# Performance work log

Measured on AMD Instinct MI355X. Metric: run time of the kernel, lower is better.

## Reference

```python
import jax, jax.numpy as jnp
import numpy as np

B, T, K = 64, 1024, 128
START, STOP = K - 2, K - 1  # tag_dictionary['<START>'], tag_dictionary['<STOP>']
NEG = -10000.0


def setup_inputs() -> dict:
    key = jax.random.key(0)
    k1, k2, k3, k4 = jax.random.split(key, 4)
    feats = jax.random.normal(k1, (B, T, K), jnp.float32)
    tags = jax.random.randint(k2, (B, T), 0, K - 2)          # real labels only
    lens = jax.random.randint(k3, (B,), 1, T + 1)            # 1 <= len <= T
    transitions = jax.random.normal(k4, (K, K), jnp.float32)
    transitions = transitions.at[START, :].set(NEG).at[:, STOP].set(NEG)
    return {"feats": feats, "tags": tags, "lens": lens, "transitions": transitions}


def _forward_alg(feats, transitions, lens):
    # feats: [B, T, K]; CRF forward (log-partition) via scan over time.
    B_, T_, K_ = feats.shape
    # init: only START position kept from feats[:, 0, :], rest -10000
    alpha0 = jnp.full((B_, K_), NEG, feats.dtype).at[:, START].set(feats[:, 0, START])

    def step(alpha, feat_i):
        # tag_var[b, s, p] = feat_i[b, s] + transitions[s, p] + alpha[b, p]
        new = feat_i + jax.scipy.special.logsumexp(alpha[:, None, :] + transitions[None, :, :], axis=2)
        return new, new

    _, alphas = jax.lax.scan(step, alpha0, jnp.swapaxes(feats[:, 1:, :], 0, 1))  # [T-1, B, K]
    all_alphas = jnp.concatenate([alpha0[None], alphas], axis=0)  # [T, B, K]; idx t-1 == forward_var[:, t]
    terminal = all_alphas[lens - 1, jnp.arange(B_)]               # [B, K]
    return jax.scipy.special.logsumexp(terminal, axis=1)          # [B]


def _score_sentence(feats, transitions, tags, lens):
    B_, T_, K_ = feats.shape
    pos = jnp.arange(T_ - 1)
    # pad_stop_tags = tags[:, 1:] with positions >= len-1 replaced by STOP
    stop_tags = jnp.where(pos[None, :] >= (lens - 1)[:, None], STOP, tags[:, 1:])
    trans_sc = transitions[stop_tags, tags[:, :-1]]               # [B, T-1]
    tmask = (pos[None, :] < (lens - 1)[:, None]).astype(feats.dtype)
    emit = jnp.take_along_axis(feats, tags[:, :, None], axis=2)[:, :, 0]  # [B, T]
    emask = (jnp.arange(T_)[None, :] < lens[:, None]).astype(feats.dtype)
    return jnp.sum(trans_sc * tmask, axis=1) + jnp.sum(emit * emask, axis=1)


def reference(feats, tags, lens, transitions):
    forward_score = _forward_alg(feats, transitions, lens)
    gold_score = _score_sentence(feats, transitions, tags, lens)
    return jnp.mean(forward_score - gold_score)
```

## Files before the change

### kernel.cpp

```cpp
#include <hip/hip_runtime.h>
#include <math.h>

#define BB 64
#define TT 1024
#define KK 128
#define START_TAG 126
#define STOP_TAG 127
#define NTHREADS 256
#define CS 64
#define EP 36

typedef float v2f __attribute__((ext_vector_type(2)));

__device__ __forceinline__ float quad_add(float x) {
  int y = __builtin_amdgcn_update_dpp(0, __float_as_int(x), 0xB1, 0xF, 0xF, true);
  x = x + __int_as_float(y);
  y = __builtin_amdgcn_update_dpp(0, __float_as_int(x), 0x4E, 0xF, 0xF, true);
  return x + __int_as_float(y);
}
__device__ __forceinline__ float quad_max(float x) {
  int y = __builtin_amdgcn_update_dpp(0, __float_as_int(x), 0xB1, 0xF, 0xF, true);
  x = fmaxf(x, __int_as_float(y));
  y = __builtin_amdgcn_update_dpp(0, __float_as_int(x), 0x4E, 0xF, 0xF, true);
  return fmaxf(x, __int_as_float(y));
}

__global__ __launch_bounds__(NTHREADS) void crf_forward(
    const float* __restrict__ feats,
    const int*   __restrict__ tags,
    const int*   __restrict__ lens,
    const float* __restrict__ trans,
    float*       __restrict__ out_pb)
{
  __shared__ float Tld[KK][KK + 1];
  __shared__ __align__(16) float ebuf[2][4 * EP];
  __shared__ float sbuf[2];
  __shared__ float maxT_lds[KK];
  __shared__ __align__(16) float Fbuf[CS * KK];
  __shared__ float wsum[NTHREADS / 64];

  const int tid = threadIdx.x;
  const int b   = blockIdx.x;
  const int q   = tid & 3;
  const int g   = tid >> 2;
  const int r0  = 2 * g;
  const int L   = lens[b];
  const float* fb = feats + (size_t)b * TT * KK;

  for (int i = tid; i < KK * KK / 4; i += NTHREADS) {
    float4 v = ((const float4*)trans)[i];
    int rr = i >> 5, cc = (i & 31) * 4;
    Tld[rr][cc] = v.x; Tld[rr][cc + 1] = v.y; Tld[rr][cc + 2] = v.z; Tld[rr][cc + 3] = v.w;
  }
  __syncthreads();

  float m0 = -INFINITY, m1 = -INFINITY;
  #pragma unroll
  for (int i = 0; i < 32; ++i) {
    m0 = fmaxf(m0, Tld[r0][q * 32 + i]);
    m1 = fmaxf(m1, Tld[r0 + 1][q * 32 + i]);
  }
  m0 = quad_max(m0);
  m1 = quad_max(m1);
  v2f Ea[16], Eb[16];
  #pragma unroll
  for (int i = 0; i < 16; ++i) {
    Ea[i][0] = __expf(Tld[r0][q * 32 + 2 * i]         - m0);
    Ea[i][1] = __expf(Tld[r0][q * 32 + 2 * i + 1]     - m0);
    Eb[i][0] = __expf(Tld[r0 + 1][q * 32 + 2 * i]     - m1);
    Eb[i][1] = __expf(Tld[r0 + 1][q * 32 + 2 * i + 1] - m1);
  }
  if (q == 0) { maxT_lds[r0] = m0; maxT_lds[r0 + 1] = m1; }

  if (tid < KK)
    ebuf[0][(tid >> 5) * EP + (tid & 31)] = (tid == START_TAG) ? 1.0f : 0.0f;
  if (tid == 0) sbuf[0] = 1.0f;
  float M = fb[START_TAG];
  __syncthreads();

  const int j0 = (tid * 32) & (KK - 1);
  float4 mTv[8];
  #pragma unroll
  for (int i = 0; i < 8; ++i) mTv[i] = ((const float4*)maxT_lds)[(j0 >> 2) + i];

  float4 pf[8];
  {
    const float4* src = (const float4*)fb;
    #pragma unroll
    for (int i = 0; i < 8; ++i) pf[i] = src[tid * 8 + i];
  }

  int p = 0;
  for (int c = 0; c * CS < L; ++c) {
    float4* Fb4 = (float4*)Fbuf;
    #pragma unroll
    for (int i = 0; i < 8; ++i) {
      float4 v = pf[i], mm = mTv[i];
      float4 o;
      o.x = __expf(v.x + mm.x); o.y = __expf(v.y + mm.y);
      o.z = __expf(v.z + mm.z); o.w = __expf(v.w + mm.w);
      Fb4[tid * 8 + i] = o;
    }
    if ((c + 1) * CS < TT) {
      const float4* src = (const float4*)(fb + (size_t)(c + 1) * CS * KK);
      #pragma unroll
      for (int i = 0; i < 8; ++i) pf[i] = src[tid * 8 + i];
    }
    __syncthreads();

    const int t_begin = (c == 0) ? 1 : c * CS;
    const int t_end   = (L < (c + 1) * CS) ? L : (c + 1) * CS;
    for (int t = t_begin; t < t_end; ++t) {
      const float* er = ebuf[p];
      float* ew = ebuf[p ^ 1];
      const float sp = sbuf[p];
      const v2f Fv = *(const v2f*)(Fbuf + (t & (CS - 1)) * KK + r0);
      float rr;
      asm("v_rcp_f32 %0, %1" : "=v"(rr) : "v"(sp));
      const float rF0 = rr * Fv[0];
      const float rF1 = rr * Fv[1];

      const v2f* ep2 = (const v2f*)(er + q * EP);
      v2f a0 = {0.f,0.f}, a1 = {0.f,0.f}, a2 = {0.f,0.f}, a3 = {0.f,0.f};
      v2f b0 = {0.f,0.f}, b1 = {0.f,0.f}, b2 = {0.f,0.f}, b3 = {0.f,0.f};
      #pragma unroll
      for (int i = 0; i < 4; ++i) {
        v2f e0 = ep2[4 * i + 0], e1 = ep2[4 * i + 1];
        v2f e2 = ep2[4 * i + 2], e3 = ep2[4 * i + 3];
        a0 += e0 * Ea[4 * i + 0];
        a1 += e1 * Ea[4 * i + 1];
        a2 += e2 * Ea[4 * i + 2];
        a3 += e3 * Ea[4 * i + 3];
        b0 += e0 * Eb[4 * i + 0];
        b1 += e1 * Eb[4 * i + 1];
        b2 += e2 * Eb[4 * i + 2];
        b3 += e3 * Eb[4 * i + 3];
      }
      v2f as = (a0 + a1) + (a2 + a3);
      v2f bs = (b0 + b1) + (b2 + b3);
      float d0 = quad_add(as[0] + as[1]);
      float d1 = quad_add(bs[0] + bs[1]);

      v2f ev; ev[0] = d0 * rF0; ev[1] = d1 * rF1;
      *(v2f*)(ew + (r0 >> 5) * EP + (r0 & 31)) = ev;
      if (g == 63) sbuf[p ^ 1] = d0;
      if (tid < 64) M += __logf(sp);
      p ^= 1;
      __syncthreads();
    }
  }

  float fwd = 0.f;
  {
    const float* efin = ebuf[p];
    if (tid < 64) {
      float sm = efin[(tid >> 5) * EP + (tid & 31)]
               + efin[((tid + 64) >> 5) * EP + ((tid + 64) & 31)];
      #pragma unroll
      for (int m = 1; m < 64; m <<= 1) sm += __shfl_xor(sm, m, 64);
      fwd = M + __logf(sm);
    }
  }

  float gold = 0.f;
  const int* tg = tags + b * TT;
  for (int t = tid; t < TT; t += NTHREADS) {
    if (t < L)     gold += fb[(size_t)t * KK + tg[t]];
    if (t < L - 1) gold += Tld[tg[t + 1]][tg[t]];
  }
  #pragma unroll
  for (int m = 1; m < 64; m <<= 1) gold += __shfl_xor(gold, m, 64);
  if ((tid & 63) == 0) wsum[tid >> 6] = gold;
  __syncthreads();
  if (tid == 0) {
    float gs = 0.f;
    #pragma unroll
    for (int w = 0; w < NTHREADS / 64; ++w) gs += wsum[w];
    out_pb[b] = fwd - gs;
  }
}

__global__ void crf_mean(const float* __restrict__ pb, float* __restrict__ out) {
  int tid = threadIdx.x;
  float v = pb[tid];
  #pragma unroll
  for (int m = 1; m < 64; m <<= 1) v += __shfl_xor(v, m, 64);
  if (tid == 0) out[0] = v * (1.0f / 64.0f);
}

extern "C" void kernel_launch(void* const* d_in, const int* in_sizes, int n_in,
                              void* d_out, int out_size, void* d_ws, size_t ws_size,
                              hipStream_t stream) {
  const float* feats = (const float*)d_in[0];
  const int*   tags  = (const int*)d_in[1];
  const int*   lens  = (const int*)d_in[2];
  const float* trans = (const float*)d_in[3];
  float* pb = (float*)d_ws;
  crf_forward<<<BB, NTHREADS, 0, stream>>>(feats, tags, lens, trans, pb);
  crf_mean<<<1, 64, 0, stream>>>(pb, (float*)d_out);
}
```

Before: 429.6 us.

## Drop transitions LDS tile, use lightweight barriers and coalesced feats prefetch

Loads transition rows directly from global memory into registers instead of staging a full 128x128 copy in LDS. Gold-score transition lookups go to global memory too. The feats chunk prefetch now uses a coalesced strided layout, so each thread needs only one vector of row maxima. __syncthreads in the serial time loop is replaced by an explicit lgkmcnt wait plus s_barrier, and only one lane per quad writes the new alpha. This aims to cut per-step barrier overhead, shared-memory footprint and setup time, at the cost of global gathers for the gold transition terms.

```diff
diff --git a/kernel.cpp b/kernel.cpp
--- a/kernel.cpp
+++ b/kernel.cpp
@@ -6,11 +6,18 @@
 #define KK 128
 #define START_TAG 126
 #define STOP_TAG 127
-#define NTHREADS 256
+#define NTH 256
 #define CS 64
 #define EP 36
 
 typedef float v2f __attribute__((ext_vector_type(2)));
+typedef float v4f __attribute__((ext_vector_type(4)));
+
+__device__ __forceinline__ void step_barrier() {
+  asm volatile("s_waitcnt lgkmcnt(0)" ::: "memory");
+  __builtin_amdgcn_s_barrier();
+  asm volatile("" ::: "memory");
+}
 
 __device__ __forceinline__ float quad_add(float x) {
   int y = __builtin_amdgcn_update_dpp(0, __float_as_int(x), 0xB1, 0xF, 0xF, true);
@@ -25,19 +32,18 @@
   return fmaxf(x, __int_as_float(y));
 }
 
-__global__ __launch_bounds__(NTHREADS) void crf_forward(
+__global__ __launch_bounds__(NTH) void crf_forward(
     const float* __restrict__ feats,
     const int*   __restrict__ tags,
     const int*   __restrict__ lens,
     const float* __restrict__ trans,
     float*       __restrict__ out_pb)
 {
-  __shared__ float Tld[KK][KK + 1];
   __shared__ __align__(16) float ebuf[2][4 * EP];
   __shared__ float sbuf[2];
-  __shared__ float maxT_lds[KK];
+  __shared__ __align__(16) float maxT_lds[KK];
   __shared__ __align__(16) float Fbuf[CS * KK];
-  __shared__ float wsum[NTHREADS / 64];
+  __shared__ float wsum[NTH / 64];
 
   const int tid = threadIdx.x;
   const int b   = blockIdx.x;
@@ -47,28 +53,25 @@
   const int L   = lens[b];
   const float* fb = feats + (size_t)b * TT * KK;
 
-  for (int i = tid; i < KK * KK / 4; i += NTHREADS) {
-    float4 v = ((const float4*)trans)[i];
-    int rr = i >> 5, cc = (i & 31) * 4;
-    Tld[rr][cc] = v.x; Tld[rr][cc + 1] = v.y; Tld[rr][cc + 2] = v.z; Tld[rr][cc + 3] = v.w;
-  }
-  __syncthreads();
-
+  v2f Ea[16], Eb[16];
   float m0 = -INFINITY, m1 = -INFINITY;
-  #pragma unroll
-  for (int i = 0; i < 32; ++i) {
-    m0 = fmaxf(m0, Tld[r0][q * 32 + i]);
-    m1 = fmaxf(m1, Tld[r0 + 1][q * 32 + i]);
+  {
+    const float* t0 = trans + (size_t)r0 * KK + q * 32;
+    const float* t1 = t0 + KK;
+    #pragma unroll
+    for (int i = 0; i < 16; ++i) {
+      Ea[i] = *(const v2f*)(t0 + 2 * i);
+      Eb[i] = *(const v2f*)(t1 + 2 * i);
+      m0 = fmaxf(m0, fmaxf(Ea[i][0], Ea[i][1]));
+      m1 = fmaxf(m1, fmaxf(Eb[i][0], Eb[i][1]));
+    }
   }
   m0 = quad_max(m0);
   m1 = quad_max(m1);
-  v2f Ea[16], Eb[16];
   #pragma unroll
   for (int i = 0; i < 16; ++i) {
-    Ea[i][0] = __expf(Tld[r0][q * 32 + 2 * i]         - m0);
-    Ea[i][1] = __expf(Tld[r0][q * 32 + 2 * i + 1]     - m0);
-    Eb[i][0] = __expf(Tld[r0 + 1][q * 32 + 2 * i]     - m1);
-    Eb[i][1] = __expf(Tld[r0 + 1][q * 32 + 2 * i + 1] - m1);
+    Ea[i][0] = __expf(Ea[i][0] - m0); Ea[i][1] = __expf(Ea[i][1] - m0);
+    Eb[i][0] = __expf(Eb[i][0] - m1); Eb[i][1] = __expf(Eb[i][1] - m1);
   }
   if (q == 0) { maxT_lds[r0] = m0; maxT_lds[r0 + 1] = m1; }
 
@@ -76,65 +79,61 @@
     ebuf[0][(tid >> 5) * EP + (tid & 31)] = (tid == START_TAG) ? 1.0f : 0.0f;
   if (tid == 0) sbuf[0] = 1.0f;
   float M = fb[START_TAG];
-  __syncthreads();
-
-  const int j0 = (tid * 32) & (KK - 1);
-  float4 mTv[8];
-  #pragma unroll
-  for (int i = 0; i < 8; ++i) mTv[i] = ((const float4*)maxT_lds)[(j0 >> 2) + i];
 
   float4 pf[8];
   {
-    const float4* src = (const float4*)fb;
-    #pragma unroll
-    for (int i = 0; i < 8; ++i) pf[i] = src[tid * 8 + i];
-  }
+    const float4* s4 = (const float4*)fb;
+    #pragma unroll
+    for (int i = 0; i < 8; ++i) pf[i] = s4[i * NTH + tid];
+  }
+
+  step_barrier();
+
+  const v4f mTv = *(const v4f*)(maxT_lds + (tid & 31) * 4);
 
   int p = 0;
   for (int c = 0; c * CS < L; ++c) {
     float4* Fb4 = (float4*)Fbuf;
     #pragma unroll
     for (int i = 0; i < 8; ++i) {
-      float4 v = pf[i], mm = mTv[i];
+      float4 v = pf[i];
       float4 o;
-      o.x = __expf(v.x + mm.x); o.y = __expf(v.y + mm.y);
-      o.z = __expf(v.z + mm.z); o.w = __expf(v.w + mm.w);
-      Fb4[tid * 8 + i] = o;
+      o.x = __expf(v.x + mTv[0]); o.y = __expf(v.y + mTv[1]);
+      o.z = __expf(v.z + mTv[2]); o.w = __expf(v.w + mTv[3]);
+      Fb4[i * NTH + tid] = o;
     }
     if ((c + 1) * CS < TT) {
-      const float4* src = (const float4*)(fb + (size_t)(c + 1) * CS * KK);
+      const float4* s4 = (const float4*)(fb + (size_t)(c + 1) * CS * KK);
       #pragma unroll
-      for (int i = 0; i < 8; ++i) pf[i] = src[tid * 8 + i];
-    }
-    __syncthreads();
-
-    const int t_begin = (c == 0) ? 1 : c * CS;
-    const int t_end   = (L < (c + 1) * CS) ? L : (c + 1) * CS;
-    for (int t = t_begin; t < t_end; ++t) {
+      for (int i = 0; i < 8; ++i) pf[i] = s4[i * NTH + tid];
+    }
+    step_barrier();
+
+    const int t_end = (L < (c + 1) * CS) ? L : (c + 1) * CS;
+    for (int t = (c == 0) ? 1 : c * CS; t < t_end; ++t) {
       const float* er = ebuf[p];
       float* ew = ebuf[p ^ 1];
       const float sp = sbuf[p];
       const v2f Fv = *(const v2f*)(Fbuf + (t & (CS - 1)) * KK + r0);
-      float rr;
-      asm("v_rcp_f32 %0, %1" : "=v"(rr) : "v"(sp));
+      float rr; asm("v_rcp_f32 %0, %1" : "=v"(rr) : "v"(sp));
       const float rF0 = rr * Fv[0];
       const float rF1 = rr * Fv[1];
 
-      const v2f* ep2 = (const v2f*)(er + q * EP);
+      const v2f* e2 = (const v2f*)(er + q * EP);
       v2f a0 = {0.f,0.f}, a1 = {0.f,0.f}, a2 = {0.f,0.f}, a3 = {0.f,0.f};
       v2f b0 = {0.f,0.f}, b1 = {0.f,0.f}, b2 = {0.f,0.f}, b3 = {0.f,0.f};
       #pragma unroll
       for (int i = 0; i < 4; ++i) {
-        v2f e0 = ep2[4 * i + 0], e1 = ep2[4 * i + 1];
-        v2f e2 = ep2[4 * i + 2], e3 = ep2[4 * i + 3];
-        a0 += e0 * Ea[4 * i + 0];
-        a1 += e1 * Ea[4 * i + 1];
-        a2 += e2 * Ea[4 * i + 2];
-        a3 += e3 * Ea[4 * i + 3];
-        b0 += e0 * Eb[4 * i + 0];
-        b1 += e1 * Eb[4 * i + 1];
-        b2 += e2 * Eb[4 * i + 2];
-        b3 += e3 * Eb[4 * i + 3];
+        v2f ea0 = e2[4 * i + 0], ea1 = e2[4 * i + 1];
+        v2f ea2 = e2[4 * i + 2], ea3 = e2[4 * i + 3];
+        a0 += ea0 * Ea[4 * i + 0];
+        a1 += ea1 * Ea[4 * i + 1];
+        a2 += ea2 * Ea[4 * i + 2];
+        a3 += ea3 * Ea[4 * i + 3];
+        b0 += ea0 * Eb[4 * i + 0];
+        b1 += ea1 * Eb[4 * i + 1];
+        b2 += ea2 * Eb[4 * i + 2];
+        b3 += ea3 * Eb[4 * i + 3];
       }
       v2f as = (a0 + a1) + (a2 + a3);
       v2f bs = (b0 + b1) + (b2 + b3);
@@ -142,11 +141,12 @@
       float d1 = quad_add(bs[0] + bs[1]);
 
       v2f ev; ev[0] = d0 * rF0; ev[1] = d1 * rF1;
-      *(v2f*)(ew + (r0 >> 5) * EP + (r0 & 31)) = ev;
-      if (g == 63) sbuf[p ^ 1] = d0;
+      if (q == 0)
+        *(v2f*)(ew + (r0 >> 5) * EP + (r0 & 31)) = ev;
+      if (tid == 252) sbuf[p ^ 1] = d0;
       if (tid < 64) M += __logf(sp);
       p ^= 1;
-      __syncthreads();
+      step_barrier();
     }
   }
 
@@ -162,21 +162,21 @@
     }
   }
 
-  float gold = 0.f;
+  float gg = 0.f;
   const int* tg = tags + b * TT;
-  for (int t = tid; t < TT; t += NTHREADS) {
-    if (t < L)     gold += fb[(size_t)t * KK + tg[t]];
-    if (t < L - 1) gold += Tld[tg[t + 1]][tg[t]];
+  for (int t = tid; t < TT; t += NTH) {
+    if (t < L)     gg += fb[(size_t)t * KK + tg[t]];
+    if (t < L - 1) gg += trans[(size_t)tg[t + 1] * KK + tg[t]];
   }
   #pragma unroll
-  for (int m = 1; m < 64; m <<= 1) gold += __shfl_xor(gold, m, 64);
-  if ((tid & 63) == 0) wsum[tid >> 6] = gold;
-  __syncthreads();
+  for (int m = 1; m < 64; m <<= 1) gg += __shfl_xor(gg, m, 64);
+  if ((tid & 63) == 0) wsum[tid >> 6] = gg;
+  step_barrier();
   if (tid == 0) {
-    float gs = 0.f;
-    #pragma unroll
-    for (int w = 0; w < NTHREADS / 64; ++w) gs += wsum[w];
-    out_pb[b] = fwd - gs;
+    float gold = 0.f;
+    #pragma unroll
+    for (int w = 0; w < NTH / 64; ++w) gold += wsum[w];
+    out_pb[b] = fwd - gold;
   }
 }
 
@@ -196,6 +196,6 @@
   const int*   lens  = (const int*)d_in[2];
   const float* trans = (const float*)d_in[3];
   float* pb = (float*)d_ws;
-  crf_forward<<<BB, NTHREADS, 0, stream>>>(feats, tags, lens, trans, pb);
+  crf_forward<<<BB, NTH, 0, stream>>>(feats, tags, lens, trans, pb);
   crf_mean<<<1, 64, 0, stream>>>(pb, (float*)d_out);
 }
```

Result: no change. 435.4 us (+1.4%).
